# Performance work log

Hardware: AMD Instinct MI355X
Metric: run time of the kernel (lower is better)

The kernel has to match this reference:

```python
import jax, jax.numpy as jnp
import numpy as np

N = 50000   # nodes
E = 800000  # edges
D = 128     # feature width (in_feats == hidden dims)
LN_EPS = 1e-5


def _degrees(src, dst, n):
    ones = jnp.ones(src.shape[0], dtype=jnp.float32)
    deg_out = jax.ops.segment_sum(ones, src, num_segments=n)
    deg_in = jax.ops.segment_sum(ones, dst, num_segments=n)
    # DGL norm='both' clamps degrees to min 1
    return jnp.maximum(deg_out, 1.0), jnp.maximum(deg_in, 1.0)


def _graph_conv(h, src, dst, inv_sqrt_out, inv_sqrt_in, W, b):
    # DGL GraphConv, norm='both': D^{-1/2} A^T D^{-1/2} X W + b
    h = h * inv_sqrt_out[:, None]                       # pre-normalize by src out-degree
    msgs = h[src]                                       # [E, D] gather
    agg = jax.ops.segment_sum(msgs, dst, num_segments=N)  # scatter-add to dst
    agg = agg * inv_sqrt_in[:, None]                    # post-normalize by dst in-degree
    return agg @ W + b


def _layer_norm(x, gamma, beta):
    mu = jnp.mean(x, axis=-1, keepdims=True)
    var = jnp.mean((x - mu) ** 2, axis=-1, keepdims=True)
    return (x - mu) * jax.lax.rsqrt(var + LN_EPS) * gamma + beta


def setup_inputs() -> dict:
    key = jax.random.key(0)
    ks = jax.random.split(key, 8)
    features = jax.random.normal(ks[0], (N, D), dtype=jnp.float32)
    src = jax.random.randint(ks[1], (E,), 0, N, dtype=jnp.int64)
    dst = jax.random.randint(ks[2], (E,), 0, N, dtype=jnp.int64)
    scale = 1.0 / np.sqrt(D)
    W1 = jax.random.normal(ks[3], (D, D), dtype=jnp.float32) * scale
    b1 = jnp.zeros((D,), dtype=jnp.float32)
    g1 = jnp.ones((D,), dtype=jnp.float32)
    be1 = jnp.zeros((D,), dtype=jnp.float32)
    W2 = jax.random.normal(ks[4], (D, D), dtype=jnp.float32) * scale
    b2 = jnp.zeros((D,), dtype=jnp.float32)
    g2 = jnp.ones((D,), dtype=jnp.float32)
    be2 = jnp.zeros((D,), dtype=jnp.float32)
    return {"features": features, "src": src, "dst": dst,
            "W1": W1, "b1": b1, "g1": g1, "be1": be1,
            "W2": W2, "b2": b2, "g2": g2, "be2": be2}


def reference(features, src, dst, W1, b1, g1, be1, W2, b2, g2, be2):
    deg_out, deg_in = _degrees(src, dst, N)
    iso = jax.lax.rsqrt(deg_out)
    isi = jax.lax.rsqrt(deg_in)
    # layer 1: GraphConv -> LayerNorm -> ReLU (dropout p=0, eval mode)
    h = _graph_conv(features, src, dst, iso, isi, W1, b1)
    h = jax.nn.relu(_layer_norm(h, g1, be1))
    # layer 2
    h = _graph_conv(h, src, dst, iso, isi, W2, b2)
    h = jax.nn.relu(_layer_norm(h, g2, be2))
    return h
```

## Files before the change

### kernel.cpp

```cpp
#include <hip/hip_runtime.h>
#include <stdint.h>

#define NN 50000
#define DD 128
#define EE 800000
#define LN_EPS 1e-5f
#define SCAN_BLOCKS ((NN + 255) / 256)
#define ROWS 32
#define ASTRIDE 136

#define CH 256
#define EC (EE / CH)
#define NP8 50000
#define NW (NP8 / 4)

typedef __attribute__((ext_vector_type(8))) short bf8_t;
typedef __attribute__((ext_vector_type(4))) float f32x4;

static __device__ __forceinline__ unsigned short f2bf(float f) {
    unsigned u = __float_as_uint(f);
    u += 0x7FFFu + ((u >> 16) & 1u);
    return (unsigned short)(u >> 16);
}

#define BF16ACC(u) do { \
    acc[0] += __uint_as_float((u).x << 16); \
    acc[1] += __uint_as_float((u).x & 0xffff0000u); \
    acc[2] += __uint_as_float((u).y << 16); \
    acc[3] += __uint_as_float((u).y & 0xffff0000u); \
    acc[4] += __uint_as_float((u).z << 16); \
    acc[5] += __uint_as_float((u).z & 0xffff0000u); \
    acc[6] += __uint_as_float((u).w << 16); \
    acc[7] += __uint_as_float((u).w & 0xffff0000u); \
} while (0)

__global__ __launch_bounds__(256) void hist_kernel(
    const int* __restrict__ src, const int* __restrict__ dst,
    unsigned char* __restrict__ epos8,
    unsigned int* __restrict__ histI, unsigned int* __restrict__ histO) {
    __shared__ unsigned int lh[NW];
    int tid = threadIdx.x;
    int c = blockIdx.x;
    int e0 = c * EC, e1 = e0 + EC;

    for (int w = tid; w < NW; w += 256) lh[w] = 0;
    __syncthreads();
    for (int e = e0 + tid; e < e1; e += 256) {
        int d = dst[e];
        int f = (d & 3) * 8;
        unsigned old = atomicAdd(&lh[d >> 2], 1u << f);
        epos8[e] = (unsigned char)(old >> f);
    }
    __syncthreads();
    {
        unsigned int* o = histI + (size_t)c * NW;
        for (int w = tid; w < NW; w += 256) o[w] = lh[w];
    }
    __syncthreads();

    for (int w = tid; w < NW; w += 256) lh[w] = 0;
    __syncthreads();
    for (int e = e0 + tid; e < e1; e += 256) {
        int d = src[e];
        atomicAdd(&lh[d >> 2], 1u << ((d & 3) * 8));
    }
    __syncthreads();
    {
        unsigned int* o = histO + (size_t)c * NW;
        for (int w = tid; w < NW; w += 256) o[w] = lh[w];
    }
}

__global__ __launch_bounds__(256) void sum_kernel(
    unsigned char* __restrict__ histI8,
    const unsigned char* __restrict__ histO8,
    int* __restrict__ cntI, float* __restrict__ iso, float* __restrict__ isi,
    int* __restrict__ bsum) {
    __shared__ int s[256];
    int tid = threadIdx.x;
    int n = blockIdx.x * 256 + tid;

    int ci = 0, co = 0;
    if (n < NN) {
#pragma unroll 8
        for (int c = 0; c < CH; c++) {
            size_t idx = (size_t)c * NP8 + n;
            unsigned char v = histI8[idx];
            histI8[idx] = (unsigned char)ci;
            ci += v;
            co += histO8[idx];
        }
        iso[n] = rsqrtf(fmaxf((float)co, 1.0f));
        isi[n] = rsqrtf(fmaxf((float)ci, 1.0f));
        cntI[n] = ci;
    }
    s[tid] = (n < NN) ? ci : 0;
    __syncthreads();
    for (int off = 128; off > 0; off >>= 1) {
        if (tid < off) s[tid] += s[tid + off];
        __syncthreads();
    }
    if (tid == 0) bsum[blockIdx.x] = s[0];
}

__global__ __launch_bounds__(256) void scanC_kernel(
    const int* __restrict__ cnt, const int* __restrict__ bsum,
    int* __restrict__ rowptr,
    const float* __restrict__ feat, const float* __restrict__ iso,
    unsigned short* __restrict__ hb) {
    __shared__ int s[256];
    __shared__ int base_s;
    __shared__ float iso_s[256];
    int tid = threadIdx.x;
    int i = blockIdx.x * 256 + tid;

    int bv = (tid < SCAN_BLOCKS && tid < blockIdx.x) ? bsum[tid] : 0;
    s[tid] = bv;
    __syncthreads();
    for (int off = 128; off > 0; off >>= 1) {
        if (tid < off) s[tid] += s[tid + off];
        __syncthreads();
    }
    if (tid == 0) base_s = s[0];
    __syncthreads();
    int base = base_s;

    iso_s[tid] = (i < NN) ? iso[i] : 1.f;
    __syncthreads();

    int v = (i < NN) ? cnt[i] : 0;
    s[tid] = v;
    __syncthreads();
    for (int off = 1; off < 256; off <<= 1) {
        int t = (tid >= off) ? s[tid - off] : 0;
        __syncthreads();
        s[tid] += t;
        __syncthreads();
    }
    if (i < NN) rowptr[i] = base + s[tid] - v;
    if (blockIdx.x == 0 && tid == 0) rowptr[NN] = EE;

    int rr = tid >> 5;
    int q = tid & 31;
    int row0 = blockIdx.x * 256;
#pragma unroll 4
    for (int it = 0; it < 32; it++) {
        int r = it * 8 + rr;
        int row = row0 + r;
        if (row < NN) {
            float sc = iso_s[r];
            float4 fv = ((const float4*)feat)[(size_t)row * 32 + q];
            ushort4 o;
            o.x = f2bf(fv.x * sc); o.y = f2bf(fv.y * sc);
            o.z = f2bf(fv.z * sc); o.w = f2bf(fv.w * sc);
            ((ushort4*)hb)[(size_t)row * 32 + q] = o;
        }
    }
}

__global__ void fill_kernel(const int* __restrict__ src, const int* __restrict__ dst,
                            const unsigned char* __restrict__ epos8,
                            const unsigned char* __restrict__ choff8,
                            const int* __restrict__ rowptr, int* __restrict__ csr,
                            const float* __restrict__ W1, const float* __restrict__ W2,
                            unsigned short* __restrict__ wbt1, unsigned short* __restrict__ wbt2) {
    int e = blockIdx.x * blockDim.x + threadIdx.x;
    if (e < EE) {
        int d = dst[e];
        int c = e / EC;
        int pos = rowptr[d] + (int)choff8[(size_t)c * NP8 + d] + (int)epos8[e];
        csr[pos] = src[e];
    }
    if (blockIdx.x < 128) {
        int idx = (blockIdx.x & 63) * 256 + threadIdx.x;
        const float* W = (blockIdx.x < 64) ? W1 : W2;
        unsigned short* wt = (blockIdx.x < 64) ? wbt1 : wbt2;
        int k = idx >> 7, n = idx & 127;
        wt[n * 128 + k] = f2bf(W[idx]);
    }
}

template <int OUTMODE>
__global__ __launch_bounds__(256) void fused_layer(
    const unsigned short* __restrict__ hb, const int* __restrict__ csr,
    const int* __restrict__ rowptr, const float* __restrict__ isi,
    const float* __restrict__ iso,
    const unsigned short* __restrict__ wbt, const float* __restrict__ b,
    const float* __restrict__ g, const float* __restrict__ be,
    float* __restrict__ outf, unsigned short* __restrict__ outb) {
    __shared__ unsigned short Asb[ROWS][ASTRIDE];
    __shared__ float redS[4][16], redSS[4][16];

    int tid = threadIdx.x;
    int node0 = blockIdx.x * ROWS;
    int w = tid >> 6;
    int lane = tid & 63;
    int quad = lane >> 4;
    int l = lane & 15;

    {
        int sub = (tid >> 4) & 3;
#pragma unroll
        for (int p = 0; p < 2; p++) {
            int r = w * 8 + p * 4 + sub;
            int n = node0 + r;
            float acc[8];
#pragma unroll
            for (int i = 0; i < 8; i++) acc[i] = 0.f;
            if (n < NN) {
                int beg = rowptr[n];
                int end = rowptr[n + 1];
                int j = beg;
                for (; j + 7 < end; j += 8) {
                    int s0 = csr[j];     int s1 = csr[j + 1];
                    int s2 = csr[j + 2]; int s3 = csr[j + 3];
                    int s4 = csr[j + 4]; int s5 = csr[j + 5];
                    int s6 = csr[j + 6]; int s7 = csr[j + 7];
                    uint4 u0 = ((const uint4*)(hb + (size_t)s0 * DD))[l];
                    uint4 u1 = ((const uint4*)(hb + (size_t)s1 * DD))[l];
                    uint4 u2 = ((const uint4*)(hb + (size_t)s2 * DD))[l];
                    uint4 u3 = ((const uint4*)(hb + (size_t)s3 * DD))[l];
                    uint4 u4 = ((const uint4*)(hb + (size_t)s4 * DD))[l];
                    uint4 u5 = ((const uint4*)(hb + (size_t)s5 * DD))[l];
                    uint4 u6 = ((const uint4*)(hb + (size_t)s6 * DD))[l];
                    uint4 u7 = ((const uint4*)(hb + (size_t)s7 * DD))[l];
                    BF16ACC(u0); BF16ACC(u1); BF16ACC(u2); BF16ACC(u3);
                    BF16ACC(u4); BF16ACC(u5); BF16ACC(u6); BF16ACC(u7);
                }
                for (; j < end; j++) {
                    int s0 = csr[j];
                    uint4 u0 = ((const uint4*)(hb + (size_t)s0 * DD))[l];
                    BF16ACC(u0);
                }
            }
            uint4 pk;
            pk.x = (unsigned)f2bf(acc[0]) | ((unsigned)f2bf(acc[1]) << 16);
            pk.y = (unsigned)f2bf(acc[2]) | ((unsigned)f2bf(acc[3]) << 16);
            pk.z = (unsigned)f2bf(acc[4]) | ((unsigned)f2bf(acc[5]) << 16);
            pk.w = (unsigned)f2bf(acc[6]) | ((unsigned)f2bf(acc[7]) << 16);
            *(uint4*)&Asb[r][l * 8] = pk;
        }
    }
    __syncthreads();

    int rt = w & 1;
    int ch = w >> 1;

    bf8_t af[4];
#pragma unroll
    for (int kb = 0; kb < 4; kb++)
        af[kb] = *(bf8_t*)&Asb[rt * 16 + l][kb * 32 + quad * 8];

    f32x4 acc[4];
#pragma unroll
    for (int tc = 0; tc < 4; tc++) acc[tc] = (f32x4){0.f, 0.f, 0.f, 0.f};

#pragma unroll
    for (int tc = 0; tc < 4; tc++) {
        int n = ch * 64 + tc * 16 + l;
#pragma unroll
        for (int kb = 0; kb < 4; kb++) {
            bf8_t bfr = *(const bf8_t*)&wbt[(size_t)n * 128 + kb * 32 + quad * 8];
            acc[tc] = __builtin_amdgcn_mfma_f32_16x16x32_bf16(af[kb], bfr, acc[tc], 0, 0, 0);
        }
    }

    float bb[4], ggv[4], bev[4];
    int cbase = ch * 64 + l;
#pragma unroll
    for (int tc = 0; tc < 4; tc++) {
        int c = cbase + tc * 16;
        bb[tc] = b[c]; ggv[tc] = g[c]; bev[tc] = be[c];
    }

    float s[4], ss[4];
#pragma unroll
    for (int i = 0; i < 4; i++) {
        int n = node0 + rt * 16 + quad * 4 + i;
        float isin = (n < NN) ? isi[n] : 1.f;
        s[i] = 0.f; ss[i] = 0.f;
#pragma unroll
        for (int tc = 0; tc < 4; tc++) {
            float v = acc[tc][i] * isin + bb[tc];
            acc[tc][i] = v;
            s[i] += v; ss[i] += v * v;
        }
    }
#pragma unroll
    for (int i = 0; i < 4; i++) {
#pragma unroll
        for (int m = 1; m <= 8; m <<= 1) {
            s[i] += __shfl_xor(s[i], m);
            ss[i] += __shfl_xor(ss[i], m);
        }
    }
    if (l == 0) {
#pragma unroll
        for (int i = 0; i < 4; i++) {
            redS[w][quad * 4 + i] = s[i];
            redSS[w][quad * 4 + i] = ss[i];
        }
    }
    __syncthreads();

#pragma unroll
    for (int i = 0; i < 4; i++) {
        int r = quad * 4 + i;
        float S  = redS[w][r]  + redS[w ^ 2][r];
        float SS = redSS[w][r] + redSS[w ^ 2][r];
        float mu = S * (1.f / 128.f);
        float var = SS * (1.f / 128.f) - mu * mu;
        float rstd = rsqrtf(var + LN_EPS);
        int n = node0 + rt * 16 + r;
        if (n < NN) {
            float isov = (OUTMODE == 1) ? iso[n] : 0.f;
            size_t base = (size_t)n * DD;
#pragma unroll
            for (int tc = 0; tc < 4; tc++) {
                float o = fmaxf((acc[tc][i] - mu) * rstd * ggv[tc] + bev[tc], 0.f);
                int c = cbase + tc * 16;
                if (OUTMODE == 0) {
                    outf[base + c] = o;
                } else {
                    outb[base + c] = f2bf(o * isov);
                }
            }
        }
    }
}

static inline char* alignp(char* p, size_t a) {
    return (char*)(((uintptr_t)p + a - 1) & ~(uintptr_t)(a - 1));
}

extern "C" void kernel_launch(void* const* d_in, const int* in_sizes, int n_in,
                              void* d_out, int out_size, void* d_ws, size_t ws_size,
                              hipStream_t stream) {
    const float* features = (const float*)d_in[0];
    const int*   src      = (const int*)d_in[1];
    const int*   dst      = (const int*)d_in[2];
    const float* W1  = (const float*)d_in[3];
    const float* b1  = (const float*)d_in[4];
    const float* g1  = (const float*)d_in[5];
    const float* be1 = (const float*)d_in[6];
    const float* W2  = (const float*)d_in[7];
    const float* b2  = (const float*)d_in[8];
    const float* g2  = (const float*)d_in[9];
    const float* be2 = (const float*)d_in[10];
    float* out = (float*)d_out;

    char* p = (char*)d_ws;
    int* cntI = (int*)p;                 p = alignp(p + NN * 4, 256);
    int* rowptr = (int*)p;               p = alignp(p + (NN + 1) * 4, 256);
    int* bsum = (int*)p;                 p = alignp(p + SCAN_BLOCKS * 4, 256);
    int* csr = (int*)p;                  p = alignp(p + (size_t)EE * 4, 256);
    float* iso = (float*)p;              p = alignp(p + NN * 4, 256);
    float* isi = (float*)p;              p = alignp(p + NN * 4, 256);
    unsigned short* hb1 = (unsigned short*)p;  p = alignp(p + (size_t)NN * DD * 2, 256);
    unsigned short* hb2 = (unsigned short*)p;  p = alignp(p + (size_t)NN * DD * 2, 256);
    unsigned short* wbt1 = (unsigned short*)p; p = alignp(p + DD * DD * 2, 256);
    unsigned short* wbt2 = (unsigned short*)p; p = alignp(p + DD * DD * 2, 256);
    unsigned char* epos8 = (unsigned char*)p;  p = alignp(p + EE, 256);

    unsigned char* histI8 = (unsigned char*)hb2;
    unsigned char* histO8 = (unsigned char*)hb1;

    hist_kernel<<<CH, 256, 0, stream>>>(src, dst, epos8,
                                        (unsigned int*)histI8, (unsigned int*)histO8);
    sum_kernel<<<SCAN_BLOCKS, 256, 0, stream>>>(histI8, histO8, cntI, iso, isi, bsum);
    scanC_kernel<<<SCAN_BLOCKS, 256, 0, stream>>>(cntI, bsum, rowptr, features, iso, hb1);
    fill_kernel<<<(EE + 255) / 256, 256, 0, stream>>>(src, dst, epos8, histI8,
                                                      rowptr, csr, W1, W2, wbt1, wbt2);

    const int fblocks = (NN + ROWS - 1) / ROWS;
    fused_layer<1><<<fblocks, 256, 0, stream>>>(hb1, csr, rowptr, isi, iso,
                                                wbt1, b1, g1, be1, nullptr, hb2);
    fused_layer<0><<<fblocks, 256, 0, stream>>>(hb2, csr, rowptr, isi, iso,
                                                wbt2, b2, g2, be2, out, nullptr);
}
```

Measured before the change: 266.2 us.

## Halve rows per block in fused layer and split MFMA columns across four waves

Each block of the fused GraphConv+LayerNorm kernel now handles 16 nodes instead of 32, one node per 16-thread group, which doubles the grid to 3125 blocks. Each of the four waves computes a 16x32 slice of the output. The LayerNorm row reduction therefore sums partials from all four waves. Because 50000 is divisible by 16, the bounds checks are removed. The goal is more blocks and shorter per-block gather tails for better load balance and latency hiding, at the cost of loading the weight matrix twice as often per node.

```diff
diff --git a/kernel.cpp b/kernel.cpp
--- a/kernel.cpp
+++ b/kernel.cpp
@@ -6,7 +6,7 @@
 #define EE 800000
 #define LN_EPS 1e-5f
 #define SCAN_BLOCKS ((NN + 255) / 256)
-#define ROWS 32
+#define ROWS 16
 #define ASTRIDE 136
 
 #define CH 256
@@ -199,65 +199,56 @@
     int l = lane & 15;
 
     {
-        int sub = (tid >> 4) & 3;
-#pragma unroll
-        for (int p = 0; p < 2; p++) {
-            int r = w * 8 + p * 4 + sub;
-            int n = node0 + r;
-            float acc[8];
-#pragma unroll
-            for (int i = 0; i < 8; i++) acc[i] = 0.f;
-            if (n < NN) {
-                int beg = rowptr[n];
-                int end = rowptr[n + 1];
-                int j = beg;
-                for (; j + 7 < end; j += 8) {
-                    int s0 = csr[j];     int s1 = csr[j + 1];
-                    int s2 = csr[j + 2]; int s3 = csr[j + 3];
-                    int s4 = csr[j + 4]; int s5 = csr[j + 5];
-                    int s6 = csr[j + 6]; int s7 = csr[j + 7];
-                    uint4 u0 = ((const uint4*)(hb + (size_t)s0 * DD))[l];
-                    uint4 u1 = ((const uint4*)(hb + (size_t)s1 * DD))[l];
-                    uint4 u2 = ((const uint4*)(hb + (size_t)s2 * DD))[l];
-                    uint4 u3 = ((const uint4*)(hb + (size_t)s3 * DD))[l];
-                    uint4 u4 = ((const uint4*)(hb + (size_t)s4 * DD))[l];
-                    uint4 u5 = ((const uint4*)(hb + (size_t)s5 * DD))[l];
-                    uint4 u6 = ((const uint4*)(hb + (size_t)s6 * DD))[l];
-                    uint4 u7 = ((const uint4*)(hb + (size_t)s7 * DD))[l];
-                    BF16ACC(u0); BF16ACC(u1); BF16ACC(u2); BF16ACC(u3);
-                    BF16ACC(u4); BF16ACC(u5); BF16ACC(u6); BF16ACC(u7);
-                }
-                for (; j < end; j++) {
-                    int s0 = csr[j];
-                    uint4 u0 = ((const uint4*)(hb + (size_t)s0 * DD))[l];
-                    BF16ACC(u0);
-                }
-            }
-            uint4 pk;
-            pk.x = (unsigned)f2bf(acc[0]) | ((unsigned)f2bf(acc[1]) << 16);
-            pk.y = (unsigned)f2bf(acc[2]) | ((unsigned)f2bf(acc[3]) << 16);
-            pk.z = (unsigned)f2bf(acc[4]) | ((unsigned)f2bf(acc[5]) << 16);
-            pk.w = (unsigned)f2bf(acc[6]) | ((unsigned)f2bf(acc[7]) << 16);
-            *(uint4*)&Asb[r][l * 8] = pk;
-        }
-    }
-    __syncthreads();
-
-    int rt = w & 1;
-    int ch = w >> 1;
+        int r = tid >> 4;
+        int n = node0 + r;
+        float acc[8];
+#pragma unroll
+        for (int i = 0; i < 8; i++) acc[i] = 0.f;
+        int beg = rowptr[n];
+        int end = rowptr[n + 1];
+        int j = beg;
+        for (; j + 7 < end; j += 8) {
+            int s0 = csr[j];     int s1 = csr[j + 1];
+            int s2 = csr[j + 2]; int s3 = csr[j + 3];
+            int s4 = csr[j + 4]; int s5 = csr[j + 5];
+            int s6 = csr[j + 6]; int s7 = csr[j + 7];
+            uint4 u0 = ((const uint4*)(hb + (size_t)s0 * DD))[l];
+            uint4 u1 = ((const uint4*)(hb + (size_t)s1 * DD))[l];
+            uint4 u2 = ((const uint4*)(hb + (size_t)s2 * DD))[l];
+            uint4 u3 = ((const uint4*)(hb + (size_t)s3 * DD))[l];
+            uint4 u4 = ((const uint4*)(hb + (size_t)s4 * DD))[l];
+            uint4 u5 = ((const uint4*)(hb + (size_t)s5 * DD))[l];
+            uint4 u6 = ((const uint4*)(hb + (size_t)s6 * DD))[l];
+            uint4 u7 = ((const uint4*)(hb + (size_t)s7 * DD))[l];
+            BF16ACC(u0); BF16ACC(u1); BF16ACC(u2); BF16ACC(u3);
+            BF16ACC(u4); BF16ACC(u5); BF16ACC(u6); BF16ACC(u7);
+        }
+        for (; j < end; j++) {
+            int s0 = csr[j];
+            uint4 u0 = ((const uint4*)(hb + (size_t)s0 * DD))[l];
+            BF16ACC(u0);
+        }
+        uint4 pk;
+        pk.x = (unsigned)f2bf(acc[0]) | ((unsigned)f2bf(acc[1]) << 16);
+        pk.y = (unsigned)f2bf(acc[2]) | ((unsigned)f2bf(acc[3]) << 16);
+        pk.z = (unsigned)f2bf(acc[4]) | ((unsigned)f2bf(acc[5]) << 16);
+        pk.w = (unsigned)f2bf(acc[6]) | ((unsigned)f2bf(acc[7]) << 16);
+        *(uint4*)&Asb[r][l * 8] = pk;
+    }
+    __syncthreads();
 
     bf8_t af[4];
 #pragma unroll
     for (int kb = 0; kb < 4; kb++)
-        af[kb] = *(bf8_t*)&Asb[rt * 16 + l][kb * 32 + quad * 8];
-
-    f32x4 acc[4];
-#pragma unroll
-    for (int tc = 0; tc < 4; tc++) acc[tc] = (f32x4){0.f, 0.f, 0.f, 0.f};
-
-#pragma unroll
-    for (int tc = 0; tc < 4; tc++) {
-        int n = ch * 64 + tc * 16 + l;
+        af[kb] = *(bf8_t*)&Asb[l][kb * 32 + quad * 8];
+
+    f32x4 acc[2];
+#pragma unroll
+    for (int tc = 0; tc < 2; tc++) acc[tc] = (f32x4){0.f, 0.f, 0.f, 0.f};
+
+#pragma unroll
+    for (int tc = 0; tc < 2; tc++) {
+        int n = w * 32 + tc * 16 + l;
 #pragma unroll
         for (int kb = 0; kb < 4; kb++) {
             bf8_t bfr = *(const bf8_t*)&wbt[(size_t)n * 128 + kb * 32 + quad * 8];
@@ -265,10 +256,10 @@
         }
     }
 
-    float bb[4], ggv[4], bev[4];
-    int cbase = ch * 64 + l;
-#pragma unroll
-    for (int tc = 0; tc < 4; tc++) {
+    float bb[2], ggv[2], bev[2];
+    int cbase = w * 32 + l;
+#pragma unroll
+    for (int tc = 0; tc < 2; tc++) {
         int c = cbase + tc * 16;
         bb[tc] = b[c]; ggv[tc] = g[c]; bev[tc] = be[c];
     }
@@ -276,11 +267,11 @@
     float s[4], ss[4];
 #pragma unroll
     for (int i = 0; i < 4; i++) {
-        int n = node0 + rt * 16 + quad * 4 + i;
-        float isin = (n < NN) ? isi[n] : 1.f;
+        int n = node0 + quad * 4 + i;
+        float isin = isi[n];
         s[i] = 0.f; ss[i] = 0.f;
 #pragma unroll
-        for (int tc = 0; tc < 4; tc++) {
+        for (int tc = 0; tc < 2; tc++) {
             float v = acc[tc][i] * isin + bb[tc];
             acc[tc][i] = v;
             s[i] += v; ss[i] += v * v;
@@ -306,24 +297,22 @@
 #pragma unroll
     for (int i = 0; i < 4; i++) {
         int r = quad * 4 + i;
-        float S  = redS[w][r]  + redS[w ^ 2][r];
-        float SS = redSS[w][r] + redSS[w ^ 2][r];
+        float S  = redS[0][r] + redS[1][r] + redS[2][r] + redS[3][r];
+        float SS = redSS[0][r] + redSS[1][r] + redSS[2][r] + redSS[3][r];
         float mu = S * (1.f / 128.f);
         float var = SS * (1.f / 128.f) - mu * mu;
         float rstd = rsqrtf(var + LN_EPS);
-        int n = node0 + rt * 16 + r;
-        if (n < NN) {
-            float isov = (OUTMODE == 1) ? iso[n] : 0.f;
-            size_t base = (size_t)n * DD;
-#pragma unroll
-            for (int tc = 0; tc < 4; tc++) {
-                float o = fmaxf((acc[tc][i] - mu) * rstd * ggv[tc] + bev[tc], 0.f);
-                int c = cbase + tc * 16;
-                if (OUTMODE == 0) {
-                    outf[base + c] = o;
-                } else {
-                    outb[base + c] = f2bf(o * isov);
-                }
+        int n = node0 + r;
+        float isov = (OUTMODE == 1) ? iso[n] : 0.f;
+        size_t base = (size_t)n * DD;
+#pragma unroll
+        for (int tc = 0; tc < 2; tc++) {
+            float o = fmaxf((acc[tc][i] - mu) * rstd * ggv[tc] + bev[tc], 0.f);
+            int c = cbase + tc * 16;
+            if (OUTMODE == 0) {
+                outf[base + c] = o;
+            } else {
+                outb[base + c] = f2bf(o * isov);
             }
         }
     }
@@ -372,7 +361,7 @@
     fill_kernel<<<(EE + 255) / 256, 256, 0, stream>>>(src, dst, epos8, histI8,
                                                       rowptr, csr, W1, W2, wbt1, wbt2);
 
-    const int fblocks = (NN + ROWS - 1) / ROWS;
+    const int fblocks = NN / ROWS;
     fused_layer<1><<<fblocks, 256, 0, stream>>>(hb1, csr, rowptr, isi, iso,
                                                 wbt1, b1, g1, be1, nullptr, hb2);
     fused_layer<0><<<fblocks, 256, 0, stream>>>(hb2, csr, rowptr, isi, iso,
```

Result: faster. 255.3 us (-4.1%).
